# Performance work log

Hardware: AMD Instinct MI355X
Metric: run time of the kernel (lower is better)

## Reference

```python
import jax, jax.numpy as jnp
import numpy as np

OS_FACTOR = 1.5
DELAY = 1                      # int(floor(os_factor))
K = DELAY / OS_FACTOR          # 1 / (os_factor / delay)
B, T, I, H = 64, 16384, 1, 64


def setup_inputs() -> dict:
    key = jax.random.key(0)
    k1, k2, k3, k4, k5 = jax.random.split(key, 5)
    s = 1.0 / np.sqrt(H).astype(np.float32)  # torch RNNCell init range
    return {
        "x": jax.random.normal(k1, (B, T, I), dtype=jnp.float32),
        "W_ih": jax.random.uniform(k2, (H, I), minval=-s, maxval=s, dtype=jnp.float32),
        "W_hh": jax.random.uniform(k3, (H, H), minval=-s, maxval=s, dtype=jnp.float32),
        "b_ih": jax.random.uniform(k4, (H,), minval=-s, maxval=s, dtype=jnp.float32),
        "b_hh": jax.random.uniform(k5, (H,), minval=-s, maxval=s, dtype=jnp.float32),
    }


def reference(x, W_ih, W_hh, b_ih, b_hh):
    # Precompute the input projection for all timesteps (parallel part).
    xw = jnp.einsum("bti,hi->bth", x, W_ih) + b_ih  # [B, T, H]

    def step(h_prev, xw_t):
        # torch.nn.RNNCell(tanh): h_next = tanh(W_ih x + b_ih + W_hh h + b_hh)
        cell = jnp.tanh(xw_t + h_prev @ W_hh.T + b_hh)
        # delay-line read (delay=1 -> previous state) + fractional blend
        h = h_prev + K * (cell - h_prev)
        return h, h

    h0 = jnp.zeros((x.shape[0], W_hh.shape[0]), dtype=x.dtype)  # zero-init delay line
    h_last, states_t = jax.lax.scan(step, h0, jnp.swapaxes(xw, 0, 1))  # scan over T
    states = jnp.swapaxes(states_t, 0, 1)  # [B, T, H]
    return states, h_last[None]  # (states, h.view(1, B, H))
```

## Files before the change

### kernel.cpp

```cpp
#include <hip/hip_runtime.h>

#define T_LEN 16384
#define HDIM 64
#define BATCH 64
#define RING  128

#define KBLEND      (2.0f / 3.0f)
#define ONE_MINUS_K (1.0f / 3.0f)
#define KK          (KBLEND * ONE_MINUS_K)

#define C2    2.8853900817779268f
#define C2K   (C2 * KBLEND)
#define C2KK  (C2 * KK)

typedef _Float16 f16x8 __attribute__((ext_vector_type(8)));
typedef float    f32x4 __attribute__((ext_vector_type(4)));

__device__ __forceinline__ float lane_bcast(float v, int lane) {
    return __int_as_float(__builtin_amdgcn_readlane(__float_as_int(v), lane));
}

__global__ __launch_bounds__(2 * HDIM)
__attribute__((amdgpu_waves_per_eu(1, 1)))
void rnn_delayline_kernel(
    const float* __restrict__ x,
    const float* __restrict__ Wih,
    const float* __restrict__ Whh,
    const float* __restrict__ bih,
    const float* __restrict__ bhh,
    float* __restrict__ out_states,
    float* __restrict__ out_hlast)
{
    const int tid  = threadIdx.x;
    const int lane = tid & (HDIM - 1);
    const int b    = blockIdx.x;

    __shared__ __align__(16) _Float16 ring[RING][HDIM];
    __shared__ int flag;

    if (tid == 0) flag = 0;
    __syncthreads();

    const float* xb = x + (size_t)b * T_LEN;
    const int NCHUNK = T_LEN / HDIM;

    if (tid < HDIM) {
        f16x8 Bf[8];
        {
            const int n = lane & 15, g = lane >> 4;
            #pragma unroll
            for (int j = 0; j < 4; ++j) {
                const float* wrow = Whh + (j * 16 + n) * HDIM;
                #pragma unroll
                for (int s = 0; s < 2; ++s) {
                    const float4* wp = reinterpret_cast<const float4*>(wrow + s * 32 + g * 8);
                    float4 v0 = wp[0], v1 = wp[1];
                    Bf[j*2+s] = (f16x8){(_Float16)v0.x, (_Float16)v0.y,
                                        (_Float16)v0.z, (_Float16)v0.w,
                                        (_Float16)v1.x, (_Float16)v1.y,
                                        (_Float16)v1.z, (_Float16)v1.w};
                }
            }
        }

        const float wihC2  = C2 * Wih[lane];
        const float biasC2 = C2 * (bih[lane] + bhh[lane]);

        const int  g8    = (lane >> 4) * 8;
        const bool selLo = ((lane >> 4) & 1) != 0;
        const bool selHi = ((lane >> 4) & 2) != 0;

        float dot = 0.0f, G = 0.0f;
        float xcur = xb[lane];

        for (int c = 0; c < NCHUNK; ++c) {
            float xnext = 0.0f;
            if (c + 1 < NCHUNK) xnext = xb[(size_t)(c + 1) * HDIM + lane];
            const int sbase = (c & 1) * 64;

            #pragma unroll 4
            for (int tt = 0; tt < HDIM; ++tt) {
                asm volatile("" : "+v"(Bf[0]), "+v"(Bf[1]), "+v"(Bf[2]), "+v"(Bf[3]),
                                  "+v"(Bf[4]), "+v"(Bf[5]), "+v"(Bf[6]), "+v"(Bf[7]));

                float xt = lane_bcast(xcur, tt);
                float cb = fmaf(xt, wihC2, biasC2) + G;

                float targ = fmaf(C2K, dot, cb);
                float e    = __builtin_amdgcn_exp2f(targ);
                float r    = __builtin_amdgcn_rcpf(1.0f + e);
                float cell = fmaf(-2.0f, r, 1.0f);

                const int slot = sbase + tt;
                ring[slot][lane] = (_Float16)cell;

                G = fmaf(ONE_MINUS_K, G, C2KK * dot);

                f16x8 a0 = *reinterpret_cast<const f16x8*>(&ring[slot][g8]);
                f16x8 a1 = *reinterpret_cast<const f16x8*>(&ring[slot][32 + g8]);

                f32x4 d0 = __builtin_amdgcn_mfma_f32_16x16x32_f16(a0, Bf[0], (f32x4){0,0,0,0}, 0, 0, 0);
                f32x4 d1 = __builtin_amdgcn_mfma_f32_16x16x32_f16(a0, Bf[2], (f32x4){0,0,0,0}, 0, 0, 0);
                f32x4 d2 = __builtin_amdgcn_mfma_f32_16x16x32_f16(a0, Bf[4], (f32x4){0,0,0,0}, 0, 0, 0);
                f32x4 d3 = __builtin_amdgcn_mfma_f32_16x16x32_f16(a0, Bf[6], (f32x4){0,0,0,0}, 0, 0, 0);
                d0 = __builtin_amdgcn_mfma_f32_16x16x32_f16(a1, Bf[1], d0, 0, 0, 0);
                d1 = __builtin_amdgcn_mfma_f32_16x16x32_f16(a1, Bf[3], d1, 0, 0, 0);
                d2 = __builtin_amdgcn_mfma_f32_16x16x32_f16(a1, Bf[5], d2, 0, 0, 0);
                d3 = __builtin_amdgcn_mfma_f32_16x16x32_f16(a1, Bf[7], d3, 0, 0, 0);

                float t01 = selLo ? d1[0] : d0[0];
                float t23 = selLo ? d3[0] : d2[0];
                dot = selHi ? t23 : t01;
            }

            xcur = xnext;
            if (lane == 0)
                __hip_atomic_store(&flag, c + 1, __ATOMIC_RELEASE,
                                   __HIP_MEMORY_SCOPE_WORKGROUP);
        }
    } else {
        float h = 0.0f;
        float* outp = out_states + (size_t)b * T_LEN * HDIM + lane;

        for (int c = 0; c < NCHUNK; ++c) {
            while (__hip_atomic_load(&flag, __ATOMIC_ACQUIRE,
                                     __HIP_MEMORY_SCOPE_WORKGROUP) <= c) {
                __builtin_amdgcn_s_sleep(2);
            }
            const int sbase = (c & 1) * 64;
            #pragma unroll 4
            for (int tt = 0; tt < HDIM; ++tt) {
                float cell = (float)ring[sbase + tt][lane];
                h = fmaf(KBLEND, cell - h, h);
                *outp = h;
                outp += HDIM;
            }
        }
        out_hlast[b * HDIM + lane] = h;
    }
}

extern "C" void kernel_launch(void* const* d_in, const int* in_sizes, int n_in,
                              void* d_out, int out_size, void* d_ws, size_t ws_size,
                              hipStream_t stream) {
    const float* x   = (const float*)d_in[0];
    const float* Wih = (const float*)d_in[1];
    const float* Whh = (const float*)d_in[2];
    const float* bih = (const float*)d_in[3];
    const float* bhh = (const float*)d_in[4];

    float* out_states = (float*)d_out;
    float* out_hlast  = out_states + (size_t)BATCH * T_LEN * HDIM;

    rnn_delayline_kernel<<<dim3(BATCH), dim3(2 * HDIM), 0, stream>>>(
        x, Wih, Whh, bih, bhh, out_states, out_hlast);
}
```

Baseline: 2.331 ms.

## Store sigmoid instead of tanh in ring and fold affine into bias

The compute wave now writes r = 1/(1+e) to the ring instead of cell = 1-2r. The affine map 1-2r is folded algebraically into the recurrence through a precomputed row sum of W_hh, and the consumer wave reconstructs cell. The next step's input term and G update are computed while the MFMAs are in flight, and the two K-halves use independent MFMAs summed afterwards rather than a chained accumulate. Together these shorten the serial dependency chain per timestep, at the cost of slightly different fp16 rounding, since r rather than cell is quantised.

```diff
diff --git a/kernel.cpp b/kernel.cpp
--- a/kernel.cpp
+++ b/kernel.cpp
@@ -9,9 +9,11 @@
 #define ONE_MINUS_K (1.0f / 3.0f)
 #define KK          (KBLEND * ONE_MINUS_K)
 
-#define C2    2.8853900817779268f
-#define C2K   (C2 * KBLEND)
-#define C2KK  (C2 * KK)
+#define C2     2.8853900817779268f
+#define C2K    (C2 * KBLEND)
+#define C2KK   (C2 * KK)
+#define N2C2K  (-2.0f * C2K)
+#define N2C2KK (-2.0f * C2KK)
 
 typedef _Float16 f16x8 __attribute__((ext_vector_type(8)));
 typedef float    f32x4 __attribute__((ext_vector_type(4)));
@@ -66,11 +68,22 @@
         const float wihC2  = C2 * Wih[lane];
         const float biasC2 = C2 * (bih[lane] + bhh[lane]);
 
+        float Wsum = 0.0f;
+        #pragma unroll 16
+        for (int k = 0; k < HDIM; ++k)
+            Wsum += (float)(_Float16)Whh[lane * HDIM + k];
+
+        const float cWsum   = C2KK * Wsum;
+        const float biasC2W = biasC2 + C2K * Wsum;
+
         const int  g8    = (lane >> 4) * 8;
         const bool selLo = ((lane >> 4) & 1) != 0;
         const bool selHi = ((lane >> 4) & 2) != 0;
 
-        float dot = 0.0f, G = 0.0f;
+        float G = 0.0f;
+        float dotm = 0.5f * Wsum;
+        float cbW  = fmaf(xb[0], wihC2, biasC2W);
+
         float xcur = xb[lane];
 
         for (int c = 0; c < NCHUNK; ++c) {
@@ -83,34 +96,39 @@
                 asm volatile("" : "+v"(Bf[0]), "+v"(Bf[1]), "+v"(Bf[2]), "+v"(Bf[3]),
                                   "+v"(Bf[4]), "+v"(Bf[5]), "+v"(Bf[6]), "+v"(Bf[7]));
 
-                float xt = lane_bcast(xcur, tt);
-                float cb = fmaf(xt, wihC2, biasC2) + G;
-
-                float targ = fmaf(C2K, dot, cb);
+                float targ = fmaf(N2C2K, dotm, cbW);
                 float e    = __builtin_amdgcn_exp2f(targ);
-                float r    = __builtin_amdgcn_rcpf(1.0f + e);
-                float cell = fmaf(-2.0f, r, 1.0f);
+                float rr   = __builtin_amdgcn_rcpf(1.0f + e);
 
                 const int slot = sbase + tt;
-                ring[slot][lane] = (_Float16)cell;
-
-                G = fmaf(ONE_MINUS_K, G, C2KK * dot);
+                ring[slot][lane] = (_Float16)rr;
 
                 f16x8 a0 = *reinterpret_cast<const f16x8*>(&ring[slot][g8]);
                 f16x8 a1 = *reinterpret_cast<const f16x8*>(&ring[slot][32 + g8]);
+                __builtin_amdgcn_sched_barrier(0);
 
-                f32x4 d0 = __builtin_amdgcn_mfma_f32_16x16x32_f16(a0, Bf[0], (f32x4){0,0,0,0}, 0, 0, 0);
-                f32x4 d1 = __builtin_amdgcn_mfma_f32_16x16x32_f16(a0, Bf[2], (f32x4){0,0,0,0}, 0, 0, 0);
-                f32x4 d2 = __builtin_amdgcn_mfma_f32_16x16x32_f16(a0, Bf[4], (f32x4){0,0,0,0}, 0, 0, 0);
-                f32x4 d3 = __builtin_amdgcn_mfma_f32_16x16x32_f16(a0, Bf[6], (f32x4){0,0,0,0}, 0, 0, 0);
-                d0 = __builtin_amdgcn_mfma_f32_16x16x32_f16(a1, Bf[1], d0, 0, 0, 0);
-                d1 = __builtin_amdgcn_mfma_f32_16x16x32_f16(a1, Bf[3], d1, 0, 0, 0);
-                d2 = __builtin_amdgcn_mfma_f32_16x16x32_f16(a1, Bf[5], d2, 0, 0, 0);
-                d3 = __builtin_amdgcn_mfma_f32_16x16x32_f16(a1, Bf[7], d3, 0, 0, 0);
+                G = fmaf(N2C2KK, dotm, fmaf(ONE_MINUS_K, G, cWsum));
+                float xsl = (tt == HDIM - 1) ? xnext : xcur;
+                float xt1 = lane_bcast(xsl, (tt + 1) & (HDIM - 1));
+                cbW = fmaf(xt1, wihC2, biasC2W) + G;
 
-                float t01 = selLo ? d1[0] : d0[0];
-                float t23 = selLo ? d3[0] : d2[0];
-                dot = selHi ? t23 : t01;
+                const f32x4 z = (f32x4){0.0f, 0.0f, 0.0f, 0.0f};
+                f32x4 d0a = __builtin_amdgcn_mfma_f32_16x16x32_f16(a0, Bf[0], z, 0, 0, 0);
+                f32x4 d1a = __builtin_amdgcn_mfma_f32_16x16x32_f16(a0, Bf[2], z, 0, 0, 0);
+                f32x4 d2a = __builtin_amdgcn_mfma_f32_16x16x32_f16(a0, Bf[4], z, 0, 0, 0);
+                f32x4 d3a = __builtin_amdgcn_mfma_f32_16x16x32_f16(a0, Bf[6], z, 0, 0, 0);
+                f32x4 d0b = __builtin_amdgcn_mfma_f32_16x16x32_f16(a1, Bf[1], z, 0, 0, 0);
+                f32x4 d1b = __builtin_amdgcn_mfma_f32_16x16x32_f16(a1, Bf[3], z, 0, 0, 0);
+                f32x4 d2b = __builtin_amdgcn_mfma_f32_16x16x32_f16(a1, Bf[5], z, 0, 0, 0);
+                f32x4 d3b = __builtin_amdgcn_mfma_f32_16x16x32_f16(a1, Bf[7], z, 0, 0, 0);
+
+                float ta01 = selLo ? d1a[0] : d0a[0];
+                float ta23 = selLo ? d3a[0] : d2a[0];
+                float ta   = selHi ? ta23 : ta01;
+                float tb01 = selLo ? d1b[0] : d0b[0];
+                float tb23 = selLo ? d3b[0] : d2b[0];
+                float tb   = selHi ? tb23 : tb01;
+                dotm = ta + tb;
             }
 
             xcur = xnext;
@@ -130,7 +148,8 @@
             const int sbase = (c & 1) * 64;
             #pragma unroll 4
             for (int tt = 0; tt < HDIM; ++tt) {
-                float cell = (float)ring[sbase + tt][lane];
+                float rr   = (float)ring[sbase + tt][lane];
+                float cell = fmaf(-2.0f, rr, 1.0f);
                 h = fmaf(KBLEND, cell - h, h);
                 *outp = h;
                 outp += HDIM;
```

Result: slower. 2.487 ms (+6.7%).
